# Optimization experiments

Hardware: AMD Instinct MI355X
Metric: run time of the kernel (lower is better)

The kernel has to match this reference:

```python
import jax, jax.numpy as jnp
import numpy as np

N_EMBD = 512
N_HEAD = 8


def setup_inputs() -> dict:
    key = jax.random.key(0)
    k_x, k_aw, k_ab, k_pw, k_pb = jax.random.split(key, 5)
    B, T, E = 4, 2048, N_EMBD
    s = 1.0 / np.sqrt(E)
    return {
        "x": jax.random.normal(k_x, (B, T, E), dtype=jnp.float32),
        # torch Linear weight is [out, in]; store transposed for x @ W
        "c_attn_w": jax.random.uniform(k_aw, (E, 3 * E), jnp.float32, -s, s),
        "c_attn_b": jax.random.uniform(k_ab, (3 * E,), jnp.float32, -s, s),
        "c_proj_w": jax.random.uniform(k_pw, (E, E), jnp.float32, -s, s),
        "c_proj_b": jax.random.uniform(k_pb, (E,), jnp.float32, -s, s),
    }


def reference(x, c_attn_w, c_attn_b, c_proj_w, c_proj_b):
    B, T, E = x.shape
    H = N_HEAD
    D = E // H
    qkv = x @ c_attn_w + c_attn_b                      # [B,T,3E]
    q, k, v = jnp.split(qkv, 3, axis=2)
    # [B,T,E] -> [B,H,T,D]
    q = q.reshape(B, T, H, D).transpose(0, 2, 1, 3)
    k = k.reshape(B, T, H, D).transpose(0, 2, 1, 3)
    v = v.reshape(B, T, H, D).transpose(0, 2, 1, 3)
    scale = 1.0 / np.sqrt(D).astype(np.float32)
    scores = jnp.einsum("bhqd,bhkd->bhqk", q, k) * scale
    causal = jnp.tril(jnp.ones((T, T), dtype=bool))    # [T,T]
    scores = jnp.where(causal, scores, -jnp.inf)
    attn = jax.nn.softmax(scores, axis=-1)             # [B,H,T,T]
    y = jnp.einsum("bhqk,bhkd->bhqd", attn, v)         # [B,H,T,D]
    y = y.transpose(0, 2, 1, 3).reshape(B, T, E)
    return y @ c_proj_w + c_proj_b
```

## Files before the change

### kernel.cpp

```cpp
#include <hip/hip_runtime.h>
#include <math.h>

#define N_EMBD 512
#define N_HEAD 8
#define SEQ_T  2048
#define BATCH  4
#define QK_LD  1024

typedef __attribute__((ext_vector_type(8))) short bf16x8;
typedef __attribute__((ext_vector_type(4))) float f32x4;

#define CL 0.18033688f

__device__ __forceinline__ unsigned short f2bf(float f) {
    union { float f; unsigned int u; } x; x.f = f;
    return (unsigned short)((x.u + 0x7FFFu + ((x.u >> 16) & 1u)) >> 16);
}
__device__ __forceinline__ unsigned pack_trunc(float a, float b) {
    union { float f; unsigned u; } x, y; x.f = a; y.f = b;
    return __builtin_amdgcn_perm(y.u, x.u, 0x07060302u);
}
__device__ __forceinline__ bf16x8 scale_frag(bf16x8 v, float c) {
    bf16x8 r;
    #pragma unroll
    for (int i = 0; i < 8; ++i) {
        union { unsigned u; float f; } x;
        x.u = ((unsigned)(unsigned short)v[i]) << 16;
        r[i] = (short)f2bf(x.f * c);
    }
    return r;
}

__global__ __launch_bounds__(256) void prep(
    const float* __restrict__ w1, unsigned short* __restrict__ w1t,
    const float* __restrict__ w2, unsigned short* __restrict__ w2t)
{
    __shared__ float t[32][33];
    const int bx = blockIdx.x, tid = threadIdx.x;
    const float* W; unsigned short* Wt; int N, tt, nb;
    if (bx < 768) { tt = bx;       W = w1; Wt = w1t; N = 1536; nb = 48; }
    else          { tt = bx - 768; W = w2; Wt = w2t; N = 512;  nb = 16; }
    const int n0 = (tt % nb) * 32, k0 = (tt / nb) * 32;
    const int tx = tid & 31, ty = tid >> 5;
    #pragma unroll
    for (int i = 0; i < 4; ++i)
        t[ty + i * 8][tx] = W[(size_t)(k0 + ty + i * 8) * N + n0 + tx];
    __syncthreads();
    #pragma unroll
    for (int i = 0; i < 4; ++i)
        Wt[(size_t)(n0 + ty + i * 8) * 512 + k0 + tx] = f2bf(t[tx][ty + i * 8]);
}

template <int BM, int BN, bool CVT_A, int OMODE>
__global__ __launch_bounds__(256) void gemm_mfma(
    const void* __restrict__ Asrc,
    const unsigned short* __restrict__ Bt,
    const float* __restrict__ bias,
    void* __restrict__ C, unsigned short* __restrict__ Cv,
    int N, int K, int xcdRows)
{
    constexpr int WMT = BM / 32, WNT = BN / 32;
    constexpr int SA = BM * 8 / 256, SB = BN * 8 / 256;
    __shared__ unsigned short As[BM * 64];
    __shared__ unsigned short Bs[BN * 64];

    const int tid  = threadIdx.x;
    const int wave = tid >> 6, lane = tid & 63;
    const int low  = lane & 15, quad = lane >> 4;
    const int wm   = (wave & 1) * (BM / 2), wn = (wave >> 1) * (BN / 2);

    const int xcd    = blockIdx.x & 7;
    const int within = blockIdx.x >> 3;
    const int rowBlk = xcd * xcdRows + (within % xcdRows);
    const int colBlk = within / xcdRows;
    const int row0 = rowBlk * BM, col0 = colBlk * BN;

    size_t a_src[SA]; int a_dst[SA];
    #pragma unroll
    for (int s = 0; s < SA; ++s) {
        const int p = tid + 256 * s;
        const int m = p >> 3, q = p & 7;
        a_src[s] = (size_t)(row0 + m) * K + q * 8;
        a_dst[s] = m * 64 + (q ^ (m & 7)) * 8;
    }
    size_t b_src[SB]; int b_dst[SB];
    #pragma unroll
    for (int s = 0; s < SB; ++s) {
        const int p = tid + 256 * s;
        const int m = p >> 3, q = p & 7;
        b_src[s] = (size_t)(col0 + m) * K + q * 8;
        b_dst[s] = m * 64 + (q ^ (m & 7)) * 8;
    }

    f32x4 acc[WMT][WNT];
    #pragma unroll
    for (int i = 0; i < WMT; ++i)
        #pragma unroll
        for (int j = 0; j < WNT; ++j) acc[i][j] = (f32x4){0.f, 0.f, 0.f, 0.f};

    bf16x8 ar[SA], br[SB];
    const float*          af32 = (const float*)Asrc;
    const unsigned short* a16  = (const unsigned short*)Asrc;

    #pragma unroll
    for (int s = 0; s < SA; ++s) {
        if (CVT_A) {
            const float4 f0 = *(const float4*)(af32 + a_src[s]);
            const float4 f1 = *(const float4*)(af32 + a_src[s] + 4);
            union { uint4 v; bf16x8 h; } u;
            u.v.x = pack_trunc(f0.x, f0.y); u.v.y = pack_trunc(f0.z, f0.w);
            u.v.z = pack_trunc(f1.x, f1.y); u.v.w = pack_trunc(f1.z, f1.w);
            ar[s] = u.h;
        } else {
            ar[s] = *(const bf16x8*)(a16 + a_src[s]);
        }
    }
    #pragma unroll
    for (int s = 0; s < SB; ++s) br[s] = *(const bf16x8*)(Bt + b_src[s]);

    const int NIT = K >> 6;
    for (int it = 0; it < NIT; ++it) {
        __syncthreads();
        #pragma unroll
        for (int s = 0; s < SA; ++s) *(bf16x8*)&As[a_dst[s]] = ar[s];
        #pragma unroll
        for (int s = 0; s < SB; ++s) *(bf16x8*)&Bs[b_dst[s]] = br[s];
        __syncthreads();

        if (it + 1 < NIT) {
            const int ko = (it + 1) * 64;
            #pragma unroll
            for (int s = 0; s < SA; ++s) {
                if (CVT_A) {
                    const float4 f0 = *(const float4*)(af32 + a_src[s] + ko);
                    const float4 f1 = *(const float4*)(af32 + a_src[s] + ko + 4);
                    union { uint4 v; bf16x8 h; } u;
                    u.v.x = pack_trunc(f0.x, f0.y); u.v.y = pack_trunc(f0.z, f0.w);
                    u.v.z = pack_trunc(f1.x, f1.y); u.v.w = pack_trunc(f1.z, f1.w);
                    ar[s] = u.h;
                } else {
                    ar[s] = *(const bf16x8*)(a16 + a_src[s] + ko);
                }
            }
            #pragma unroll
            for (int s = 0; s < SB; ++s) br[s] = *(const bf16x8*)(Bt + b_src[s] + ko);
        }

        #pragma unroll
        for (int h = 0; h < 2; ++h) {
            bf16x8 af[WMT], bfr[WNT];
            #pragma unroll
            for (int t = 0; t < WMT; ++t)
                af[t] = *(const bf16x8*)
                    &As[(wm + t * 16 + low) * 64 + (((h * 4 + quad) ^ (low & 7)) * 8)];
            #pragma unroll
            for (int t = 0; t < WNT; ++t)
                bfr[t] = *(const bf16x8*)
                    &Bs[(wn + t * 16 + low) * 64 + (((h * 4 + quad) ^ (low & 7)) * 8)];
            #pragma unroll
            for (int i = 0; i < WMT; ++i)
                #pragma unroll
                for (int j = 0; j < WNT; ++j)
                    acc[i][j] = __builtin_amdgcn_mfma_f32_16x16x32_bf16(
                        af[i], bfr[j], acc[i][j], 0, 0, 0);
        }
    }

    float bv[WNT];
    #pragma unroll
    for (int j = 0; j < WNT; ++j) bv[j] = bias[col0 + wn + j * 16 + low];
    const bool isV = (OMODE == 2) && (col0 >= 1024);
    #pragma unroll
    for (int i = 0; i < WMT; ++i)
        #pragma unroll
        for (int r = 0; r < 4; ++r) {
            const int row = row0 + wm + i * 16 + quad * 4 + r;
            #pragma unroll
            for (int j = 0; j < WNT; ++j) {
                const int col = col0 + wn + j * 16 + low;
                const float v = acc[i][j][r] + bv[j];
                if (OMODE == 0) {
                    ((float*)C)[(size_t)row * N + col] = v;
                } else if (OMODE == 1) {
                    ((unsigned short*)C)[(size_t)row * N + col] = f2bf(v);
                } else {
                    if (isV)
                        Cv[((size_t)((row >> 11) * 512 + col - 1024) << 11)
                           + (row & 2047)] = f2bf(v);
                    else
                        ((unsigned short*)C)[(size_t)row * QK_LD + col] = f2bf(v);
                }
            }
        }
}

template<bool MASK>
__device__ __forceinline__ void qk_step(
    const bf16x8 k00, const bf16x8 k01, const bf16x8 k10, const bf16x8 k11,
    const bf16x8 (&qf)[2][2], bf16x8 (&pf)[2], float (&lp)[2],
    const int qrel0, const int koffb)
{
    #pragma unroll
    for (int qb = 0; qb < 2; ++qb) {
        f32x4 s0 = (f32x4){0.f, 0.f, 0.f, 0.f};
        f32x4 s1 = (f32x4){0.f, 0.f, 0.f, 0.f};
        s0 = __builtin_amdgcn_mfma_f32_16x16x32_bf16(k00, qf[qb][0], s0, 0, 0, 0);
        s0 = __builtin_amdgcn_mfma_f32_16x16x32_bf16(k01, qf[qb][1], s0, 0, 0, 0);
        s1 = __builtin_amdgcn_mfma_f32_16x16x32_bf16(k10, qf[qb][0], s1, 0, 0, 0);
        s1 = __builtin_amdgcn_mfma_f32_16x16x32_bf16(k11, qf[qb][1], s1, 0, 0, 0);
        float p[8];
        #pragma unroll
        for (int r = 0; r < 4; ++r) {
            float v0 = s0[r], v1 = s1[r];
            if (MASK) {
                const int qrel = qrel0 + qb * 16;
                if (koffb + r     > qrel) v0 = -1e30f;
                if (koffb + r + 4 > qrel) v1 = -1e30f;
            }
            p[r]     = __builtin_amdgcn_exp2f(v0);
            p[r + 4] = __builtin_amdgcn_exp2f(v1);
        }
        #pragma unroll
        for (int e = 0; e < 8; ++e) {
            union { float f; unsigned u; } c; c.f = p[e];
            c.u &= 0xFFFF0000u; p[e] = c.f;
        }
        lp[qb] += ((p[0] + p[1]) + (p[2] + p[3])) + ((p[4] + p[5]) + (p[6] + p[7]));
        union { uint4 v; bf16x8 h; } u;
        u.v.x = pack_trunc(p[0], p[1]); u.v.y = pack_trunc(p[2], p[3]);
        u.v.z = pack_trunc(p[4], p[5]); u.v.w = pack_trunc(p[6], p[7]);
        pf[qb] = u.h;
    }
}

__global__ __launch_bounds__(256, 2) void attn_mfma(
    const unsigned short* __restrict__ qk,
    const unsigned short* __restrict__ vT,
    unsigned short* __restrict__ y)
{
    const int bh  = blockIdx.x & 31;
    const int pa  = blockIdx.x >> 5;
    const int b   = bh >> 3, h = bh & 7;
    const int qA0 = pa * 64;
    const int qB0 = (31 - pa) * 64;
    const int nA  = pa + 1, nB = 32 - pa;
    const int tid = threadIdx.x;
    const int wave = tid >> 6, lane = tid & 63;
    const int low  = lane & 15, quad = lane >> 4;
    const int kh   = wave & 1, qh = wave >> 1;

    __shared__ float oBuf[2][64 * 66];
    __shared__ float lBuf[2][2][64];

    const size_t base = (size_t)b * SEQ_T * QK_LD + h * 64;
    const unsigned short* qp = qk + base;
    const unsigned short* kp = qk + base + 512;
    const unsigned short* vp = vT + ((size_t)(b * 512 + h * 64) << 11);

    bf16x8 qf[2][2][2];
    #pragma unroll
    for (int s = 0; s < 2; ++s) {
        const int q0 = (s ? qB0 : qA0) + qh * 32;
        #pragma unroll
        for (int qb = 0; qb < 2; ++qb) {
            const size_t qr = (size_t)(q0 + qb * 16 + low) * QK_LD;
            #pragma unroll
            for (int dh = 0; dh < 2; ++dh)
                qf[s][qb][dh] = scale_frag(
                    *(const bf16x8*)(qp + qr + dh * 32 + quad * 8), CL);
        }
    }

    const int rowperm = ((low >> 2) << 3) + (low & 3);
    const unsigned short* kbase =
        kp + (size_t)(kh * 32 + rowperm) * QK_LD + quad * 8;
    const int koffb = kh * 32 + quad * 8;
    const unsigned short* vrow = vp + (size_t)low * SEQ_T + koffb;

    bf16x8 kk[4], vv[4];
    kk[0] = *(const bf16x8*)(kbase);
    kk[1] = *(const bf16x8*)(kbase + 32);
    kk[2] = *(const bf16x8*)(kbase + 4 * QK_LD);
    kk[3] = *(const bf16x8*)(kbase + 4 * QK_LD + 32);
    #pragma unroll
    for (int t = 0; t < 4; ++t)
        vv[t] = *(const bf16x8*)(vrow + (size_t)(t * 16) * SEQ_T);

    f32x4 o[2][2][4];
    #pragma unroll
    for (int s = 0; s < 2; ++s)
        #pragma unroll
        for (int qb = 0; qb < 2; ++qb)
            #pragma unroll
            for (int t = 0; t < 4; ++t) o[s][qb][t] = (f32x4){0.f, 0.f, 0.f, 0.f};
    float lp[2][2] = {{0.f, 0.f}, {0.f, 0.f}};

    for (int kc = 0; kc < nB; ++kc) {
        bf16x8 nk[4], nv[4];
        const bool pfch = (kc + 1 < nB);
        if (pfch) {
            const unsigned short* kb = kbase + (size_t)(kc + 1) * (64 * QK_LD);
            nk[0] = *(const bf16x8*)(kb);
            nk[1] = *(const bf16x8*)(kb + 32);
            nk[2] = *(const bf16x8*)(kb + 4 * QK_LD);
            nk[3] = *(const bf16x8*)(kb + 4 * QK_LD + 32);
            const unsigned short* vb = vrow + (kc + 1) * 64;
            #pragma unroll
            for (int t = 0; t < 4; ++t)
                nv[t] = *(const bf16x8*)(vb + (size_t)(t * 16) * SEQ_T);
        }

        const int kc64 = kc * 64;
        bf16x8 pA[2], pB[2];
        const bool doA = (kc < nA);
        if (doA) {
            const int qrelA = qA0 + qh * 32 + low - kc64;
            if (kc == nA - 1)
                qk_step<true >(kk[0], kk[1], kk[2], kk[3], qf[0], pA, lp[0], qrelA, koffb);
            else
                qk_step<false>(kk[0], kk[1], kk[2], kk[3], qf[0], pA, lp[0], qrelA, koffb);
        }
        {
            const int qrelB = qB0 + qh * 32 + low - kc64;
            if (kc == nB - 1)
                qk_step<true >(kk[0], kk[1], kk[2], kk[3], qf[1], pB, lp[1], qrelB, koffb);
            else
                qk_step<false>(kk[0], kk[1], kk[2], kk[3], qf[1], pB, lp[1], qrelB, koffb);
        }

        if (doA) {
            #pragma unroll
            for (int t = 0; t < 4; ++t) {
                o[0][0][t] = __builtin_amdgcn_mfma_f32_16x16x32_bf16(pA[0], vv[t], o[0][0][t], 0, 0, 0);
                o[0][1][t] = __builtin_amdgcn_mfma_f32_16x16x32_bf16(pA[1], vv[t], o[0][1][t], 0, 0, 0);
            }
        }
        #pragma unroll
        for (int t = 0; t < 4; ++t) {
            o[1][0][t] = __builtin_amdgcn_mfma_f32_16x16x32_bf16(pB[0], vv[t], o[1][0][t], 0, 0, 0);
            o[1][1][t] = __builtin_amdgcn_mfma_f32_16x16x32_bf16(pB[1], vv[t], o[1][1][t], 0, 0, 0);
        }

        if (pfch) {
            #pragma unroll
            for (int t = 0; t < 4; ++t) { kk[t] = nk[t]; vv[t] = nv[t]; }
        }
    }

    #pragma unroll
    for (int s = 0; s < 2; ++s)
        #pragma unroll
        for (int qb = 0; qb < 2; ++qb) {
            float v = lp[s][qb];
            v += __shfl_xor(v, 16);
            v += __shfl_xor(v, 32);
            if (quad == 0) lBuf[kh][qh][(s * 2 + qb) * 16 + low] = v;
        }
    if (kh == 1) {
        #pragma unroll
        for (int s = 0; s < 2; ++s)
            #pragma unroll
            for (int qb = 0; qb < 2; ++qb)
                #pragma unroll
                for (int t = 0; t < 4; ++t)
                    #pragma unroll
                    for (int r = 0; r < 4; ++r)
                        oBuf[qh][((s * 2 + qb) * 16 + quad * 4 + r) * 66 + low + t * 16]
                            = o[s][qb][t][r];
    }
    __syncthreads();
    if (kh == 0) {
        #pragma unroll
        for (int s = 0; s < 2; ++s) {
            const int q0 = (s ? qB0 : qA0) + qh * 32;
            #pragma unroll
            for (int qb = 0; qb < 2; ++qb) {
                #pragma unroll
                for (int r = 0; r < 4; ++r) {
                    const int ri = (s * 2 + qb) * 16 + quad * 4 + r;
                    const float l = lBuf[0][qh][ri] + lBuf[1][qh][ri];
                    const float rl = 1.f / l;
                    const int qrow = q0 + qb * 16 + quad * 4 + r;
                    unsigned short* yp =
                        y + (size_t)(b * SEQ_T + qrow) * N_EMBD + h * 64 + low;
                    #pragma unroll
                    for (int t = 0; t < 4; ++t)
                        yp[t * 16] = f2bf(
                            (o[s][qb][t][r] + oBuf[qh][ri * 66 + low + t * 16]) * rl);
                }
            }
        }
    }
}

extern "C" void kernel_launch(void* const* d_in, const int* in_sizes, int n_in,
                              void* d_out, int out_size, void* d_ws, size_t ws_size,
                              hipStream_t stream)
{
    const float* x      = (const float*)d_in[0];
    const float* attn_w = (const float*)d_in[1];
    const float* attn_b = (const float*)d_in[2];
    const float* proj_w = (const float*)d_in[3];
    const float* proj_b = (const float*)d_in[4];
    float*       out    = (float*)d_out;

    char* ws = (char*)d_ws;
    unsigned short* qk_bf = (unsigned short*)(ws);
    unsigned short* vT    = (unsigned short*)(ws + 16777216);
    unsigned short* y_bf  = (unsigned short*)(ws + 25165824);
    unsigned short* w1t   = (unsigned short*)(ws + 33554432);
    unsigned short* w2t   = (unsigned short*)(ws + 35127296);

    prep<<<1024, 256, 0, stream>>>(attn_w, w1t, proj_w, w2t);

    gemm_mfma<128, 128, true, 2><<<dim3(768), 256, 0, stream>>>(
        x, w1t, attn_b, qk_bf, vT, 1536, N_EMBD, 8);

    attn_mfma<<<dim3(512), 256, 0, stream>>>(qk_bf, vT, y_bf);

    gemm_mfma<64, 128, false, 0><<<dim3(512), 256, 0, stream>>>(
        y_bf, w2t, proj_b, out, nullptr, N_EMBD, N_EMBD, 16);
}
```

Measured before the change: 166.0 us.

## Stage K/V tiles through double-buffered LDS via direct global-to-LDS loads

The attention kernel now loads each 64-key K and V tile once per block into swizzled, double-buffered shared memory using global_load_lds, instead of every wave loading its own fragments from global memory into registers. Waves then read their fragments from LDS, and a barrier per iteration guards buffer reuse. Separately, the QKV GEMM epilogue for the V part is transposed through shared memory so the column-major V layout is written with vectorized 16-byte stores rather than scattered 2-byte stores. The cost is extra barriers and LDS traffic, which may hurt occupancy at two blocks per CU.

```diff
diff --git a/kernel.cpp b/kernel.cpp
--- a/kernel.cpp
+++ b/kernel.cpp
@@ -29,6 +29,12 @@
         r[i] = (short)f2bf(x.f * c);
     }
     return r;
+}
+
+__device__ __forceinline__ void gl_lds16(const void* g, void* s) {
+    __builtin_amdgcn_global_load_lds(
+        (const __attribute__((address_space(1))) void*)g,
+        (__attribute__((address_space(3))) void*)s, 16, 0, 0);
 }
 
 __global__ __launch_bounds__(256) void prep(
@@ -61,8 +67,9 @@
 {
     constexpr int WMT = BM / 32, WNT = BN / 32;
     constexpr int SA = BM * 8 / 256, SB = BN * 8 / 256;
-    __shared__ unsigned short As[BM * 64];
-    __shared__ unsigned short Bs[BN * 64];
+    __shared__ unsigned short SM[BM * 64 + BN * 64];
+    unsigned short* As = SM;
+    unsigned short* Bs = SM + BM * 64;
 
     const int tid  = threadIdx.x;
     const int wave = tid >> 6, lane = tid & 63;
@@ -169,29 +176,54 @@
     float bv[WNT];
     #pragma unroll
     for (int j = 0; j < WNT; ++j) bv[j] = bias[col0 + wn + j * 16 + low];
+
     const bool isV = (OMODE == 2) && (col0 >= 1024);
-    #pragma unroll
-    for (int i = 0; i < WMT; ++i)
-        #pragma unroll
-        for (int r = 0; r < 4; ++r) {
-            const int row = row0 + wm + i * 16 + quad * 4 + r;
-            #pragma unroll
-            for (int j = 0; j < WNT; ++j) {
-                const int col = col0 + wn + j * 16 + low;
-                const float v = acc[i][j][r] + bv[j];
-                if (OMODE == 0) {
-                    ((float*)C)[(size_t)row * N + col] = v;
-                } else if (OMODE == 1) {
-                    ((unsigned short*)C)[(size_t)row * N + col] = f2bf(v);
-                } else {
-                    if (isV)
-                        Cv[((size_t)((row >> 11) * 512 + col - 1024) << 11)
-                           + (row & 2047)] = f2bf(v);
+    if (isV) {
+        unsigned short (*Cs)[130] = (unsigned short (*)[130])SM;
+        const int bI = row0 >> 11;
+        const int t0 = row0 & 2047;
+        const int dloc = tid >> 2, sub = tid & 3;
+        __syncthreads();
+        #pragma unroll
+        for (int p = 0; p < 2; ++p) {
+            if ((wave >> 1) == p) {
+                #pragma unroll
+                for (int i = 0; i < WMT; ++i)
+                    #pragma unroll
+                    for (int j = 0; j < WNT; ++j)
+                        #pragma unroll
+                        for (int r = 0; r < 4; ++r)
+                            Cs[j * 16 + low][wm + i * 16 + quad * 4 + r] =
+                                f2bf(acc[i][j][r] + bv[j]);
+            }
+            __syncthreads();
+            const int dglob = col0 - 1024 + p * 64 + dloc;
+            unsigned short* vb =
+                Cv + (((size_t)(bI * 512 + dglob)) << 11) + t0 + sub * 8;
+            #pragma unroll
+            for (int e = 0; e < 4; ++e)
+                *(bf16x8*)(vb + e * 32) = *(const bf16x8*)&Cs[dloc][e * 32 + sub * 8];
+            __syncthreads();
+        }
+    } else {
+        #pragma unroll
+        for (int i = 0; i < WMT; ++i)
+            #pragma unroll
+            for (int r = 0; r < 4; ++r) {
+                const int row = row0 + wm + i * 16 + quad * 4 + r;
+                #pragma unroll
+                for (int j = 0; j < WNT; ++j) {
+                    const int col = col0 + wn + j * 16 + low;
+                    const float v = acc[i][j][r] + bv[j];
+                    if (OMODE == 0)
+                        ((float*)C)[(size_t)row * N + col] = v;
+                    else if (OMODE == 1)
+                        ((unsigned short*)C)[(size_t)row * N + col] = f2bf(v);
                     else
                         ((unsigned short*)C)[(size_t)row * QK_LD + col] = f2bf(v);
                 }
             }
-        }
+    }
 }
 
 template<bool MASK>
@@ -249,8 +281,9 @@
     const int low  = lane & 15, quad = lane >> 4;
     const int kh   = wave & 1, qh = wave >> 1;
 
-    __shared__ float oBuf[2][64 * 66];
-    __shared__ float lBuf[2][2][64];
+    __shared__ char smem[34816];
+    unsigned short* KsB = (unsigned short*)smem;
+    unsigned short* VsB = (unsigned short*)smem + 8192;
 
     const size_t base = (size_t)b * SEQ_T * QK_LD + h * 64;
     const unsigned short* qp = qk + base;
@@ -271,20 +304,33 @@
         }
     }
 
-    const int rowperm = ((low >> 2) << 3) + (low & 3);
-    const unsigned short* kbase =
-        kp + (size_t)(kh * 32 + rowperm) * QK_LD + quad * 8;
+    const int r8 = lane >> 3, s8 = lane & 7;
+    const unsigned short* ksrc[2]; const unsigned short* vsrc[2]; int dst[2];
+    #pragma unroll
+    for (int ii = 0; ii < 2; ++ii) {
+        const int hs = (r8 & 3) | (ii << 2);
+        ksrc[ii] = kp + (size_t)(wave * 16 + ii * 8 + r8) * QK_LD + (s8 ^ hs) * 8;
+        vsrc[ii] = vp + ((size_t)(wave * 16 + ii * 8 + r8) << 11) + (s8 ^ hs) * 8;
+        dst[ii]  = (wave * 16 + ii * 8) * 64;
+    }
+
+    const int hkv = (low & 3) | (((low >> 2) & 1) << 2);
+    const int hvv = (low & 3) | ((low >> 3) << 2);
+    const int krow0 = kh * 32 + ((low >> 2) << 3) + (low & 3);
+    const int koffK[2][2] = {
+        { krow0 * 64 + ((quad    ) ^ hkv) * 8, krow0 * 64 + ((quad + 4) ^ hkv) * 8 },
+        { (krow0+4)*64 + ((quad  ) ^ hkv) * 8, (krow0+4)*64 + ((quad + 4) ^ hkv) * 8 } };
+    int voff[4];
+    #pragma unroll
+    for (int t = 0; t < 4; ++t)
+        voff[t] = (t * 16 + low) * 64 + ((kh * 4 + quad) ^ hvv) * 8;
     const int koffb = kh * 32 + quad * 8;
-    const unsigned short* vrow = vp + (size_t)low * SEQ_T + koffb;
-
-    bf16x8 kk[4], vv[4];
-    kk[0] = *(const bf16x8*)(kbase);
-    kk[1] = *(const bf16x8*)(kbase + 32);
-    kk[2] = *(const bf16x8*)(kbase + 4 * QK_LD);
-    kk[3] = *(const bf16x8*)(kbase + 4 * QK_LD + 32);
-    #pragma unroll
-    for (int t = 0; t < 4; ++t)
-        vv[t] = *(const bf16x8*)(vrow + (size_t)(t * 16) * SEQ_T);
+
+    #pragma unroll
+    for (int ii = 0; ii < 2; ++ii) {
+        gl_lds16(ksrc[ii], KsB + dst[ii]);
+        gl_lds16(vsrc[ii], VsB + dst[ii]);
+    }
 
     f32x4 o[2][2][4];
     #pragma unroll
@@ -295,20 +341,32 @@
             for (int t = 0; t < 4; ++t) o[s][qb][t] = (f32x4){0.f, 0.f, 0.f, 0.f};
     float lp[2][2] = {{0.f, 0.f}, {0.f, 0.f}};
 
+    __syncthreads();
+
     for (int kc = 0; kc < nB; ++kc) {
-        bf16x8 nk[4], nv[4];
-        const bool pfch = (kc + 1 < nB);
-        if (pfch) {
-            const unsigned short* kb = kbase + (size_t)(kc + 1) * (64 * QK_LD);
-            nk[0] = *(const bf16x8*)(kb);
-            nk[1] = *(const bf16x8*)(kb + 32);
-            nk[2] = *(const bf16x8*)(kb + 4 * QK_LD);
-            nk[3] = *(const bf16x8*)(kb + 4 * QK_LD + 32);
-            const unsigned short* vb = vrow + (kc + 1) * 64;
-            #pragma unroll
-            for (int t = 0; t < 4; ++t)
-                nv[t] = *(const bf16x8*)(vb + (size_t)(t * 16) * SEQ_T);
-        }
+        const int cur = kc & 1;
+        if (kc + 1 < nB) {
+            const size_t kadv = (size_t)(kc + 1) * 64 * QK_LD;
+            const int    vadv = (kc + 1) * 64;
+            const int    db   = (cur ^ 1) * 4096;
+            #pragma unroll
+            for (int ii = 0; ii < 2; ++ii) {
+                gl_lds16(ksrc[ii] + kadv, KsB + db + dst[ii]);
+                gl_lds16(vsrc[ii] + vadv, VsB + db + dst[ii]);
+            }
+        }
+
+        const unsigned short* Kc = KsB + cur * 4096;
+        const unsigned short* Vc = VsB + cur * 4096;
+        bf16x8 kf[2][2], vf[4];
+        #pragma unroll
+        for (int kt = 0; kt < 2; ++kt)
+            #pragma unroll
+            for (int dh = 0; dh < 2; ++dh)
+                kf[kt][dh] = *(const bf16x8*)&Kc[koffK[kt][dh]];
+        #pragma unroll
+        for (int t = 0; t < 4; ++t)
+            vf[t] = *(const bf16x8*)&Vc[voff[t]];
 
         const int kc64 = kc * 64;
         bf16x8 pA[2], pB[2];
@@ -316,36 +374,36 @@
         if (doA) {
             const int qrelA = qA0 + qh * 32 + low - kc64;
             if (kc == nA - 1)
-                qk_step<true >(kk[0], kk[1], kk[2], kk[3], qf[0], pA, lp[0], qrelA, koffb);
+                qk_step<true >(kf[0][0], kf[0][1], kf[1][0], kf[1][1], qf[0], pA, lp[0], qrelA, koffb);
             else
-                qk_step<false>(kk[0], kk[1], kk[2], kk[3], qf[0], pA, lp[0], qrelA, koffb);
+                qk_step<false>(kf[0][0], kf[0][1], kf[1][0], kf[1][1], qf[0], pA, lp[0], qrelA, koffb);
         }
         {
             const int qrelB = qB0 + qh * 32 + low - kc64;
             if (kc == nB - 1)
-                qk_step<true >(kk[0], kk[1], kk[2], kk[3], qf[1], pB, lp[1], qrelB, koffb);
+                qk_step<true >(kf[0][0], kf[0][1], kf[1][0], kf[1][1], qf[1], pB, lp[1], qrelB, koffb);
             else
-                qk_step<false>(kk[0], kk[1], kk[2], kk[3], qf[1], pB, lp[1], qrelB, koffb);
+                qk_step<false>(kf[0][0], kf[0][1], kf[1][0], kf[1][1], qf[1], pB, lp[1], qrelB, koffb);
         }
 
         if (doA) {
             #pragma unroll
             for (int t = 0; t < 4; ++t) {
-                o[0][0][t] = __builtin_amdgcn_mfma_f32_16x16x32_bf16(pA[0], vv[t], o[0][0][t], 0, 0, 0);
-                o[0][1][t] = __builtin_amdgcn_mfma_f32_16x16x32_bf16(pA[1], vv[t], o[0][1][t], 0, 0, 0);
+                o[0][0][t] = __builtin_amdgcn_mfma_f32_16x16x32_bf16(pA[0], vf[t], o[0][0][t], 0, 0, 0);
+                o[0][1][t] = __builtin_amdgcn_mfma_f32_16x16x32_bf16(pA[1], vf[t], o[0][1][t], 0, 0, 0);
             }
         }
         #pragma unroll
         for (int t = 0; t < 4; ++t) {
-            o[1][0][t] = __builtin_amdgcn_mfma_f32_16x16x32_bf16(pB[0], vv[t], o[1][0][t], 0, 0, 0);
-            o[1][1][t] = __builtin_amdgcn_mfma_f32_16x16x32_bf16(pB[1], vv[t], o[1][1][t], 0, 0, 0);
-        }
-
-        if (pfch) {
-            #pragma unroll
-            for (int t = 0; t < 4; ++t) { kk[t] = nk[t]; vv[t] = nv[t]; }
-        }
-    }
+            o[1][0][t] = __builtin_amdgcn_mfma_f32_16x16x32_bf16(pB[0], vf[t], o[1][0][t], 0, 0, 0);
+            o[1][1][t] = __builtin_amdgcn_mfma_f32_16x16x32_bf16(pB[1], vf[t], o[1][1][t], 0, 0, 0);
+        }
+
+        __syncthreads();
+    }
+
+    float* oB = (float*)smem;
+    float* lB = (float*)(smem + 33792);
 
     #pragma unroll
     for (int s = 0; s < 2; ++s)
@@ -354,7 +412,7 @@
             float v = lp[s][qb];
             v += __shfl_xor(v, 16);
             v += __shfl_xor(v, 32);
-            if (quad == 0) lBuf[kh][qh][(s * 2 + qb) * 16 + low] = v;
+            if (quad == 0) lB[(kh * 2 + qh) * 64 + (s * 2 + qb) * 16 + low] = v;
         }
     if (kh == 1) {
         #pragma unroll
@@ -365,8 +423,8 @@
                 for (int t = 0; t < 4; ++t)
                     #pragma unroll
                     for (int r = 0; r < 4; ++r)
-                        oBuf[qh][((s * 2 + qb) * 16 + quad * 4 + r) * 66 + low + t * 16]
-                            = o[s][qb][t][r];
+                        oB[qh * 4224 + ((s * 2 + qb) * 16 + quad * 4 + r) * 66
+                           + low + t * 16] = o[s][qb][t][r];
     }
     __syncthreads();
     if (kh == 0) {
@@ -378,7 +436,7 @@
                 #pragma unroll
                 for (int r = 0; r < 4; ++r) {
                     const int ri = (s * 2 + qb) * 16 + quad * 4 + r;
-                    const float l = lBuf[0][qh][ri] + lBuf[1][qh][ri];
+                    const float l = lB[qh * 64 + ri] + lB[128 + qh * 64 + ri];
                     const float rl = 1.f / l;
                     const int qrow = q0 + qb * 16 + quad * 4 + r;
                     unsigned short* yp =
@@ -386,7 +444,7 @@
                     #pragma unroll
                     for (int t = 0; t < 4; ++t)
                         yp[t * 16] = f2bf(
-                            (o[s][qb][t][r] + oBuf[qh][ri * 66 + low + t * 16]) * rl);
+                            (o[s][qb][t][r] + oB[qh * 4224 + ri * 66 + low + t * 16]) * rl);
                 }
             }
         }
```

After: 134.7 us. 1.23x faster.
